# Optimization experiments

Hardware: AMD Instinct MI355X
Metric: run time of the kernel (lower is better)

The kernel has to match this reference:

```python
import jax, jax.numpy as jnp
import numpy as np

B, T, C = 2, 4096, 1024
H, M, CHUNK = 16, 64, 128
D = C // H
DELTA = 1e-6


def setup_inputs() -> dict:
    key = jax.random.key(0)
    ks = jax.random.split(key, 4)
    x = jax.random.normal(ks[0], (B, T, C), dtype=jnp.float32)
    Wqkv = jax.random.normal(ks[1], (3 * C, C), dtype=jnp.float32) * 0.02
    bqkv = jnp.zeros((3 * C,), dtype=jnp.float32)
    Wout = jax.random.normal(ks[2], (C, C), dtype=jnp.float32) * 0.02
    bout = jnp.zeros((C,), dtype=jnp.float32)
    proj = jax.random.normal(ks[3], (H, D, M), dtype=jnp.float32) / np.sqrt(D)
    return {"x": x, "Wqkv": Wqkv, "bqkv": bqkv, "Wout": Wout, "bout": bout, "proj": proj}


def reference(x, Wqkv, bqkv, Wout, bout, proj):
    b, t, c = x.shape
    qkv = x @ Wqkv.T + bqkv                      # (B,T,3C)
    q, k, v = jnp.split(qkv, 3, axis=-1)
    # (B,T,C) -> (B,H,T,D)
    def to_heads(z):
        return z.reshape(b, t, H, D).transpose(0, 2, 1, 3).astype(jnp.float32)
    q, k, v = to_heads(q), to_heads(k), to_heads(v)

    nch = t // CHUNK
    # (B,H,T,D) -> (nch, B, H, Tc, D)
    def to_chunks(z):
        return z.reshape(b, H, nch, CHUNK, D).transpose(2, 0, 1, 3, 4)
    qc, kc, vc = to_chunks(q), to_chunks(k), to_chunks(v)

    mask = jnp.tril(jnp.ones((CHUNK, CHUNK), dtype=jnp.float32))

    def step(carry, inp):
        kv_state, k_state = carry                 # (B,H,M,D), (B,H,M)
        q_ch, k_ch, v_ch = inp                    # (B,H,Tc,D)
        qp = jax.nn.relu(jnp.einsum('bhtd,hdm->bhtm', q_ch, proj))
        kp = jax.nn.relu(jnp.einsum('bhtd,hdm->bhtm', k_ch, proj))
        ctx_hist = jnp.einsum('bhtm,bhmd->bhtd', qp, kv_state)
        norm_hist = jnp.einsum('bhtm,bhm->bht', qp, k_state)
        aw = jnp.einsum('bhtm,bhsm->bhts', qp, kp) * mask  # causal intra-chunk
        ctx_intra = jnp.einsum('bhts,bhsd->bhtd', aw, v_ch)
        norm_intra = aw.sum(-1)
        out = (ctx_hist + ctx_intra) / (norm_hist + norm_intra + DELTA)[..., None]
        new_kv = kv_state + jnp.einsum('bhtm,bhtd->bhmd', kp, v_ch)
        new_k = k_state + kp.sum(2)
        return (new_kv, new_k), out

    carry0 = (jnp.zeros((b, H, M, D), jnp.float32), jnp.zeros((b, H, M), jnp.float32))
    _, outs = jax.lax.scan(step, carry0, (qc, kc, vc))  # (nch,B,H,Tc,D)
    out = outs.transpose(1, 2, 0, 3, 4).reshape(b, H, t, D)  # (B,H,T,D)
    out = out.transpose(0, 2, 1, 3).reshape(b, t, c)          # (B,T,C)
    return out @ Wout.T + bout
```

## Files before the change

### kernel.cpp

```cpp
#include <hip/hip_runtime.h>
#include <stdint.h>

#define HN 16
#define DH 64
#define MF 64
#define CHK 128
#define NCH 32
#define TSEQ 4096
#define CIN 1024
#define C3 3072

typedef __attribute__((ext_vector_type(8))) short bf16x8;
typedef __attribute__((ext_vector_type(4))) float f32x4;

__device__ __forceinline__ unsigned short f2b(float f){
  union{float f;uint32_t u;} v; v.f=f;
  return (unsigned short)((v.u + 0x7fffu + ((v.u>>16)&1u))>>16);
}

#define MFMA(a,b,c) __builtin_amdgcn_mfma_f32_16x16x32_bf16(a,b,c,0,0,0)

typedef __attribute__((address_space(1))) void gbl_t;
typedef __attribute__((address_space(3))) void lds_t;
__device__ __forceinline__ void gload_lds16(const void* g, void* l){
  __builtin_amdgcn_global_load_lds((const gbl_t*)g, (lds_t*)l, 16, 0, 0);
}

__global__ __launch_bounds__(256) void cvt_kernel(const float* __restrict__ src,
                                                  unsigned short* __restrict__ dst, int n4){
  int i = blockIdx.x*256 + threadIdx.x;
  if (i >= n4) return;
  float4 v = ((const float4*)src)[i];
  uint64_t pk = (uint64_t)f2b(v.x) | ((uint64_t)f2b(v.y)<<16)
              | ((uint64_t)f2b(v.z)<<32) | ((uint64_t)f2b(v.w)<<48);
  *(uint64_t*)(dst + (size_t)i*4) = pk;
}

__global__ __launch_bounds__(256) void projt_kernel(const float* __restrict__ proj,
                                                    unsigned short* __restrict__ projT){
  int i = blockIdx.x*256 + threadIdx.x;
  if (i >= HN*DH*MF) return;
  int h = i>>12, r = i&4095, d = r>>6, m = r&63;
  projT[(h<<12) + (m<<6) + d] = f2b(proj[i]);
}

template<int OUT_BF16, int KK>
__global__ __launch_bounds__(512, 2) void gemm8p_kernel(
    const unsigned short* __restrict__ A, const unsigned short* __restrict__ Bt,
    const float* __restrict__ bias, void* __restrict__ Cout,
    int Nn, int nbN)
{
  static_assert(KK % 128 == 0, "KK multiple of 128");
  constexpr int NT = KK / 64;
  constexpr int NI = NT / 2;
  static_assert((NT & (NT-1)) == 0, "NT pow2 for wrap");

  __shared__ unsigned short sA[2*256*64];
  __shared__ unsigned short sB[2*128*64];

  int tid = threadIdx.x;
  int w = tid>>6, l = tid&63, g = l>>4, r16 = l&15;
  int wr = w>>2, wc = w&3;

  int nwg = gridDim.x;
  int qq = nwg>>3;
  int wgid = (blockIdx.x & 7)*qq + (blockIdx.x>>3);
  int brow = (wgid / nbN)<<8;
  int bcol = (wgid % nbN)<<7;

  int rofs = tid>>3;
  int cofs = ((tid&7) ^ ((tid>>3)&7))<<3;

  const unsigned short* Ab = A + (size_t)brow*KK;
  const unsigned short* Bb = Bt + (size_t)bcol*KK;
  char* sAc = (char*)sA;
  char* sBc = (char*)sB;

  f32x4 acc[8][2];
  #pragma unroll
  for (int m=0;m<8;m++)
    #pragma unroll
    for (int n=0;n<2;n++) acc[m][n] = (f32x4){0.f,0.f,0.f,0.f};

  auto stgA = [&](int buf, int half, int kt){
    int r0 = half<<7;
    const unsigned short* gp = Ab + (size_t)(r0 + rofs)*KK + (kt<<6) + cofs;
    char* lp = sAc + (buf<<15) + (r0<<7) + (tid<<4);
    gload_lds16(gp, lp);
    gload_lds16(gp + (size_t)64*KK, lp + 8192);
  };
  auto stgB = [&](int buf, int kt){
    const unsigned short* gp = Bb + (size_t)rofs*KK + (kt<<6) + cofs;
    char* lp = sBc + (buf<<14) + (tid<<4);
    gload_lds16(gp, lp);
    gload_lds16(gp + (size_t)64*KK, lp + 8192);
  };

  bf16x8 af[4][2];
  bf16x8 bfv[2][2];

#define LDA(SAB, MH) do{                                                            \
    _Pragma("unroll")                                                               \
    for (int mf_=0; mf_<4; mf_++){                                                  \
      int row_ = wr*128 + (MH)*64 + mf_*16 + r16;                                   \
      _Pragma("unroll")                                                             \
      for (int ks_=0; ks_<2; ks_++)                                                 \
        af[mf_][ks_] = *(const bf16x8*)((SAB) + row_*128 + (((ks_*4+g)^(r16&7))<<4));\
    } }while(0)
#define LDB(SBB, NH) do{                                                            \
    int row_ = wc*32 + (NH)*16 + r16;                                               \
    _Pragma("unroll")                                                               \
    for (int ks_=0; ks_<2; ks_++)                                                   \
      bfv[NH][ks_] = *(const bf16x8*)((SBB) + row_*128 + (((ks_*4+g)^(r16&7))<<4)); \
    }while(0)
#define MM(MH, NH) do{                                                              \
    __builtin_amdgcn_s_barrier();                                                   \
    __builtin_amdgcn_sched_barrier(0);                                              \
    __builtin_amdgcn_s_setprio(1);                                                  \
    _Pragma("unroll")                                                               \
    for (int mf_=0; mf_<4; mf_++)                                                   \
      _Pragma("unroll")                                                             \
      for (int ks_=0; ks_<2; ks_++)                                                 \
        acc[(MH)*4+mf_][(NH)] = MFMA(af[mf_][ks_], bfv[NH][ks_], acc[(MH)*4+mf_][(NH)]); \
    __builtin_amdgcn_s_setprio(0);                                                  \
    __builtin_amdgcn_sched_barrier(0);                                              \
    __builtin_amdgcn_s_barrier();                                                   \
    asm volatile("" ::: "memory");                                                  \
  }while(0)
#define VM2 asm volatile("s_waitcnt vmcnt(2)" ::: "memory")

  const char* a0 = sAc;
  const char* a1 = sAc + (1<<15);
  const char* b0 = sBc;
  const char* b1 = sBc + (1<<14);

  stgA(0,0,0); stgA(0,1,0); stgB(0,0);
  stgA(1,0,1);
  VM2;
  __builtin_amdgcn_s_barrier();
  asm volatile("" ::: "memory");

  for (int it=0; it<NI; ++it){
    int to  = 2*it+1;
    int tn  = (2*it+2) & (NT-1);
    int tnn = (2*it+3) & (NT-1);
    LDA(a0,0); LDB(b0,0); stgA(1,1,to);        MM(0,0);
    LDB(b0,1);            stgB(1,to);          MM(0,1);
    LDA(a0,1);            stgA(0,0,tn);        MM(1,1);
                                         VM2;  MM(1,0);
    LDA(a1,0); LDB(b1,0); stgA(0,1,tn);        MM(0,0);
    LDB(b1,1);            stgB(0,tn);          MM(0,1);
    LDA(a1,1);            stgA(1,0,tnn);       MM(1,1);
                                         VM2;  MM(1,0);
  }
#undef LDA
#undef LDB
#undef MM
#undef VM2

  #pragma unroll
  for (int n=0;n<2;n++){
    int colg = bcol + wc*32 + n*16 + r16;
    float bv = bias[colg];
    #pragma unroll
    for (int m=0;m<8;m++){
      int rowg = brow + wr*128 + (m>>2)*64 + (m&3)*16 + g*4;
      #pragma unroll
      for (int j=0;j<4;j++){
        float v = acc[m][n][j] + bv;
        if (OUT_BF16) ((unsigned short*)Cout)[(size_t)(rowg+j)*Nn + colg] = f2b(v);
        else          ((float*)Cout)[(size_t)(rowg+j)*Nn + colg] = v;
      }
    }
  }
}

__global__ __launch_bounds__(256) void chunk_stats_kernel(
    const unsigned short* __restrict__ qkvb,
    const unsigned short* __restrict__ projT,
    float* __restrict__ Sbuf, float* __restrict__ ssum)
{
  __shared__ unsigned short s_pT[64*64];
  __shared__ unsigned short s_kpT[64*128];
  __shared__ unsigned short s_vT[64*128];
  __shared__ float s_part[256];

  int bid = blockIdx.x;
  int ch = bid&31, h = (bid>>5)&15, b = bid>>9;
  int tid = threadIdx.x, w = tid>>6, l = tid&63, g = l>>4, r16 = l&15;
  int rowbase = b*TSEQ + ch*CHK;
  const unsigned short* kg = qkvb + (size_t)rowbase*C3 + CIN   + h*DH;
  const unsigned short* vg = qkvb + (size_t)rowbase*C3 + 2*CIN + h*DH;

  {
    const unsigned short* p = projT + (h<<12);
    for (int i = tid; i < 4096; i += 256){
      int m = i>>6, d = i&63;
      *(unsigned short*)((char*)s_pT + m*128 + (((d*2) ^ ((m&7)<<4)))) = p[i];
    }
  }
  for (int i = tid; i < 1024; i += 256){
    int t = i>>3, d0 = (i&7)<<3;
    bf16x8 vv = *(const bf16x8*)(vg + (size_t)t*C3 + d0);
    #pragma unroll
    for (int j=0;j<8;j++){
      int d = d0+j;
      *(unsigned short*)((char*)s_vT + d*256 + (((t*2) ^ ((d&15)<<4)))) = (unsigned short)vv[j];
    }
  }
  __syncthreads();

  f32x4 kacc[2][4];
  #pragma unroll
  for (int tr=0;tr<2;tr++)
    #pragma unroll
    for (int nc=0;nc<4;nc++) kacc[tr][nc] = (f32x4){0.f,0.f,0.f,0.f};
  #pragma unroll
  for (int ks=0; ks<2; ks++){
    bf16x8 a[2];
    #pragma unroll
    for (int tr=0;tr<2;tr++){
      int t = w*32 + tr*16 + r16;
      a[tr] = *(const bf16x8*)(kg + (size_t)t*C3 + ks*32 + g*8);
    }
    #pragma unroll
    for (int nc=0;nc<4;nc++){
      int m = nc*16 + r16;
      bf16x8 bb = *(const bf16x8*)((const char*)s_pT + m*128 + (((ks*64 + g*16) ^ ((m&7)<<4))));
      #pragma unroll
      for (int tr=0;tr<2;tr++)
        kacc[tr][nc] = MFMA(a[tr], bb, kacc[tr][nc]);
    }
  }
  #pragma unroll
  for (int nc=0;nc<4;nc++){
    float v = 0.f;
    #pragma unroll
    for (int tr=0;tr<2;tr++)
      #pragma unroll
      for (int j=0;j<4;j++){
        float x = kacc[tr][nc][j]; x = x>0.f?x:0.f;
        v += x;
        int t = w*32 + tr*16 + g*4 + j;
        int m = nc*16 + r16;
        *(unsigned short*)((char*)s_kpT + m*256 + (((t*2) ^ ((m&15)<<4)))) = f2b(x);
      }
    v += __shfl_xor(v,16); v += __shfl_xor(v,32);
    if (g==0) s_part[w*64 + nc*16 + r16] = v;
  }
  __syncthreads();

  f32x4 sacc[4];
  #pragma unroll
  for (int dc=0;dc<4;dc++) sacc[dc] = (f32x4){0.f,0.f,0.f,0.f};
  int mrow = w*16 + r16;
  #pragma unroll
  for (int ks=0; ks<4; ks++){
    bf16x8 a = *(const bf16x8*)((const char*)s_kpT + mrow*256 + (((ks*64 + g*16) ^ ((mrow&15)<<4))));
    #pragma unroll
    for (int dc=0; dc<4; dc++){
      int d = dc*16 + r16;
      bf16x8 bb = *(const bf16x8*)((const char*)s_vT + d*256 + (((ks*64 + g*16) ^ ((d&15)<<4))));
      sacc[dc] = MFMA(a, bb, sacc[dc]);
    }
  }
  float* So = Sbuf + ((size_t)((b*HN + h)*NCH + ch))*4096;
  #pragma unroll
  for (int dc=0; dc<4; dc++)
    #pragma unroll
    for (int j=0;j<4;j++)
      So[(w*16 + g*4 + j)*64 + dc*16 + r16] = sacc[dc][j];
  if (tid < 64){
    float v = s_part[tid] + s_part[64+tid] + s_part[128+tid] + s_part[192+tid];
    ssum[((size_t)((b*HN + h)*NCH + ch))*64 + tid] = v;
  }
}

__global__ __launch_bounds__(256) void scan_kernel(
  const float* __restrict__ Sbuf, const float* __restrict__ ssum,
  float* __restrict__ kvstate, float* __restrict__ kstate)
{
  int bh = blockIdx.x>>2, qd = blockIdx.x&3, tid = threadIdx.x;
  const float4* Sp = (const float4*)(Sbuf + (size_t)bh*NCH*4096);
  float4* kvp = (float4*)(kvstate + (size_t)bh*NCH*4096);
  int idx0 = (tid>>2)*16 + qd*4 + (tid&3);
  float4 acc = make_float4(0.f,0.f,0.f,0.f);
  for (int c2=0; c2<NCH; c2++){
    int idx = c2*1024 + idx0;
    float4 s = Sp[idx];
    kvp[idx] = acc;
    acc.x += s.x; acc.y += s.y; acc.z += s.z; acc.w += s.w;
  }
  if (qd==0 && tid < 64){
    float a = 0.f;
    const float* sp = ssum + (size_t)bh*NCH*64;
    float* kp2 = kstate + (size_t)bh*NCH*64;
    for (int c2=0;c2<NCH;c2++){ kp2[c2*64+tid] = a; a += sp[c2*64+tid]; }
  }
}

__global__ __launch_bounds__(256) void chunk_out_kernel(
    const unsigned short* __restrict__ qkvb,
    const unsigned short* __restrict__ projT,
    const float* __restrict__ kvstate,
    const float* __restrict__ kstate,
    unsigned short* __restrict__ attnb)
{
  __shared__ unsigned short s_qp[128*64];
  __shared__ unsigned short s_kp[128*64];
  __shared__ unsigned short s_vT[64*128];
  __shared__ unsigned short s_pa[64*64];

  int bid = blockIdx.x;
  int ch = bid&31, h=(bid>>5)&15, b=bid>>9;
  int tid=threadIdx.x, w=tid>>6, l=tid&63, g=l>>4, r16=l&15;
  int rowbase = b*TSEQ + ch*CHK;
  const unsigned short* qg = qkvb + (size_t)rowbase*C3 + h*DH;
  const unsigned short* kg = qg + CIN;
  const unsigned short* vg = qg + 2*CIN;
  const float* kvg = kvstate + ((size_t)((b*HN+h)*NCH + ch))*4096;
  const float* ksg = kstate  + ((size_t)((b*HN+h)*NCH + ch))*64;

  {
    const unsigned short* p = projT + (h<<12);
    for (int i = tid; i < 4096; i += 256){
      int m = i>>6, d = i&63;
      *(unsigned short*)((char*)s_pa + m*128 + (((d*2) ^ ((m&7)<<4)))) = p[i];
    }
  }
  for (int i = tid; i < 1024; i += 256){
    int t = i>>3, d0 = (i&7)<<3;
    bf16x8 vv = *(const bf16x8*)(vg + (size_t)t*C3 + d0);
    #pragma unroll
    for (int j=0;j<8;j++){
      int d = d0+j;
      *(unsigned short*)((char*)s_vT + d*256 + (((t*2) ^ ((d&15)<<4)))) = (unsigned short)vv[j];
    }
  }
  __syncthreads();

  f32x4 qacc[2][4];
  #pragma unroll
  for (int tr=0;tr<2;tr++)
    #pragma unroll
    for (int nc=0;nc<4;nc++) qacc[tr][nc] = (f32x4){0.f,0.f,0.f,0.f};
  #pragma unroll
  for (int ks=0; ks<2; ks++){
    bf16x8 a[2];
    #pragma unroll
    for (int tr=0;tr<2;tr++){
      int t = w*32 + tr*16 + r16;
      a[tr] = *(const bf16x8*)(qg + (size_t)t*C3 + ks*32 + g*8);
    }
    #pragma unroll
    for (int nc=0;nc<4;nc++){
      int m = nc*16 + r16;
      bf16x8 bb = *(const bf16x8*)((const char*)s_pa + m*128 + (((ks*64 + g*16) ^ ((m&7)<<4))));
      #pragma unroll
      for (int tr=0;tr<2;tr++)
        qacc[tr][nc] = MFMA(a[tr], bb, qacc[tr][nc]);
    }
  }
  float nh[2][4];
  #pragma unroll
  for (int tr=0;tr<2;tr++)
    #pragma unroll
    for (int j=0;j<4;j++) nh[tr][j] = 0.f;
  #pragma unroll
  for (int nc=0;nc<4;nc++){
    float ksv = ksg[nc*16 + r16];
    #pragma unroll
    for (int tr=0;tr<2;tr++)
      #pragma unroll
      for (int j=0;j<4;j++){
        float x = qacc[tr][nc][j]; x = x>0.f?x:0.f;
        nh[tr][j] += x*ksv;
        int t = w*32 + tr*16 + g*4 + j;
        int m = nc*16 + r16;
        *(unsigned short*)((char*)s_qp + t*128 + (((m*2) ^ ((t&7)<<4)))) = f2b(x);
      }
  }
  f32x4 kacc[2][4];
  #pragma unroll
  for (int tr=0;tr<2;tr++)
    #pragma unroll
    for (int nc=0;nc<4;nc++) kacc[tr][nc] = (f32x4){0.f,0.f,0.f,0.f};
  #pragma unroll
  for (int ks=0; ks<2; ks++){
    bf16x8 a[2];
    #pragma unroll
    for (int tr=0;tr<2;tr++){
      int t = w*32 + tr*16 + r16;
      a[tr] = *(const bf16x8*)(kg + (size_t)t*C3 + ks*32 + g*8);
    }
    #pragma unroll
    for (int nc=0;nc<4;nc++){
      int m = nc*16 + r16;
      bf16x8 bb = *(const bf16x8*)((const char*)s_pa + m*128 + (((ks*64 + g*16) ^ ((m&7)<<4))));
      #pragma unroll
      for (int tr=0;tr<2;tr++)
        kacc[tr][nc] = MFMA(a[tr], bb, kacc[tr][nc]);
    }
  }
  #pragma unroll
  for (int nc=0;nc<4;nc++)
    #pragma unroll
    for (int tr=0;tr<2;tr++)
      #pragma unroll
      for (int j=0;j<4;j++){
        float x = kacc[tr][nc][j]; x = x>0.f?x:0.f;
        int t = w*32 + tr*16 + g*4 + j;
        int m = nc*16 + r16;
        *(unsigned short*)((char*)s_kp + t*128 + (((m*2) ^ ((t&7)<<4)))) = f2b(x);
      }
  __syncthreads();

  f32x4 ctx[2][4];
  float ni[2][4];
  #pragma unroll
  for (int tr=0;tr<2;tr++){
    #pragma unroll
    for (int dc=0;dc<4;dc++) ctx[tr][dc] = (f32x4){0.f,0.f,0.f,0.f};
    #pragma unroll
    for (int j=0;j<4;j++) ni[tr][j] = 0.f;
  }

  for (int sb=0; sb<4; sb++){
    f32x4 aw[2][2];
    #pragma unroll
    for (int tr=0;tr<2;tr++)
      #pragma unroll
      for (int sc=0;sc<2;sc++) aw[tr][sc] = (f32x4){0.f,0.f,0.f,0.f};
    #pragma unroll
    for (int ks=0; ks<2; ks++){
      bf16x8 a[2];
      #pragma unroll
      for (int tr=0;tr<2;tr++){
        int t = w*32 + tr*16 + r16;
        a[tr] = *(const bf16x8*)((const char*)s_qp + t*128 + (((ks*64 + g*16) ^ ((t&7)<<4))));
      }
      #pragma unroll
      for (int sc=0;sc<2;sc++){
        int s = sb*32 + sc*16 + r16;
        bf16x8 bb = *(const bf16x8*)((const char*)s_kp + s*128 + (((ks*64 + g*16) ^ ((s&7)<<4))));
        #pragma unroll
        for (int tr=0;tr<2;tr++)
          aw[tr][sc] = MFMA(a[tr], bb, aw[tr][sc]);
      }
    }
    #pragma unroll
    for (int tr=0;tr<2;tr++)
      #pragma unroll
      for (int sc=0;sc<2;sc++)
        #pragma unroll
        for (int j=0;j<4;j++){
          int t = w*32 + tr*16 + g*4 + j;
          int s = sb*32 + sc*16 + r16;
          float x = (s<=t)? aw[tr][sc][j] : 0.f;
          ni[tr][j] += x;
          int sl = sc*16 + r16;
          *(unsigned short*)((char*)s_pa + t*64 + (((sl*2) ^ ((t&3)<<4)))) = f2b(x);
        }
    __syncthreads();
    #pragma unroll
    for (int tr=0;tr<2;tr++){
      int t = w*32 + tr*16 + r16;
      bf16x8 a2 = *(const bf16x8*)((const char*)s_pa + t*64 + (((g*16) ^ ((t&3)<<4))));
      #pragma unroll
      for (int dc=0;dc<4;dc++){
        int d = dc*16 + r16;
        bf16x8 bb = *(const bf16x8*)((const char*)s_vT + d*256 + (((sb*64 + g*16) ^ ((d&15)<<4))));
        ctx[tr][dc] = MFMA(a2, bb, ctx[tr][dc]);
      }
    }
    __syncthreads();
  }

  #pragma unroll
  for (int ks=0; ks<2; ks++){
    bf16x8 a[2];
    #pragma unroll
    for (int tr=0;tr<2;tr++){
      int t = w*32 + tr*16 + r16;
      a[tr] = *(const bf16x8*)((const char*)s_qp + t*128 + (((ks*64 + g*16) ^ ((t&7)<<4))));
    }
    #pragma unroll
    for (int dc=0;dc<4;dc++){
      bf16x8 bb;
      #pragma unroll
      for (int i=0;i<8;i++)
        bb[i] = (short)f2b(kvg[(ks*32 + g*8 + i)*64 + dc*16 + r16]);
      #pragma unroll
      for (int tr=0;tr<2;tr++)
        ctx[tr][dc] = MFMA(a[tr], bb, ctx[tr][dc]);
    }
  }

  float nrm[2][4];
  #pragma unroll
  for (int tr=0;tr<2;tr++)
    #pragma unroll
    for (int j=0;j<4;j++){
      float v = nh[tr][j] + ni[tr][j];
      v += __shfl_xor(v,1); v += __shfl_xor(v,2);
      v += __shfl_xor(v,4); v += __shfl_xor(v,8);
      nrm[tr][j] = v + 1e-6f;
    }

  #pragma unroll
  for (int tr=0;tr<2;tr++)
    #pragma unroll
    for (int dc=0;dc<4;dc++)
      #pragma unroll
      for (int j=0;j<4;j++){
        int t = w*32 + tr*16 + g*4 + j;
        int d = dc*16 + r16;
        attnb[(size_t)(rowbase + t)*CIN + h*DH + d] = f2b(ctx[tr][dc][j] / nrm[tr][j]);
      }
}

extern "C" void kernel_launch(void* const* d_in, const int* in_sizes, int n_in,
                              void* d_out, int out_size, void* d_ws, size_t ws_size,
                              hipStream_t stream)
{
  const float* x    = (const float*)d_in[0];
  const float* Wqkv = (const float*)d_in[1];
  const float* bqkv = (const float*)d_in[2];
  const float* Wout = (const float*)d_in[3];
  const float* bout = (const float*)d_in[4];
  const float* proj = (const float*)d_in[5];

  char* ws = (char*)d_ws;
  unsigned short* xb     = (unsigned short*)(ws + 0);
  unsigned short* attnb  = (unsigned short*)(ws + 0);
  unsigned short* wqkvb  = (unsigned short*)(ws + 16777216);
  float*          ssum   = (float*)(ws + 16777216);
  float*          kstate = (float*)(ws + 17039360);
  unsigned short* qkvb   = (unsigned short*)(ws + 23068672);
  unsigned short* woutb  = (unsigned short*)(ws + 73400320);
  unsigned short* projTb = (unsigned short*)(ws + 75497472);
  float*          Sbuf   = (float*)(ws + 75628544);
  float*          kvstate= (float*)(ws + 92405760);

  cvt_kernel<<<8192, 256, 0, stream>>>(x, xb, 2097152);
  cvt_kernel<<<3072, 256, 0, stream>>>(Wqkv, wqkvb, 786432);
  cvt_kernel<<<1024, 256, 0, stream>>>(Wout, woutb, 262144);
  projt_kernel<<<256, 256, 0, stream>>>(proj, projTb);

  gemm8p_kernel<1,1024><<<768, 512, 0, stream>>>(xb, wqkvb, bqkv, qkvb, 3072, 24);

  chunk_stats_kernel<<<1024, 256, 0, stream>>>(qkvb, projTb, Sbuf, ssum);
  scan_kernel<<<128, 256, 0, stream>>>(Sbuf, ssum, kvstate, kstate);
  chunk_out_kernel<<<1024, 256, 0, stream>>>(qkvb, projTb, kvstate, kstate, attnb);

  gemm8p_kernel<0,1024><<<256, 512, 0, stream>>>(attnb, woutb, bout, d_out, 1024, 8);
}
```

Before: 164.5 us.

## Widen GEMM block tile to 256x256 for more operand reuse

The GEMM block tile grows from 256x128 to 256x256. Each wave now computes a 128x64 output with 32 accumulator fragments, and the B staging is split into two halves with a reworked load/wait schedule. The goal is higher arithmetic intensity per LDS load and less global traffic for B. In exchange the kernel uses more registers and LDS, which hurts occupancy, and the grid halves (384 and 128 blocks), leaving the output projection with fewer blocks than the 256 CUs.

```diff
diff --git a/kernel.cpp b/kernel.cpp
--- a/kernel.cpp
+++ b/kernel.cpp
@@ -56,7 +56,7 @@
   static_assert((NT & (NT-1)) == 0, "NT pow2 for wrap");
 
   __shared__ unsigned short sA[2*256*64];
-  __shared__ unsigned short sB[2*128*64];
+  __shared__ unsigned short sB[2*256*64];
 
   int tid = threadIdx.x;
   int w = tid>>6, l = tid&63, g = l>>4, r16 = l&15;
@@ -66,7 +66,7 @@
   int qq = nwg>>3;
   int wgid = (blockIdx.x & 7)*qq + (blockIdx.x>>3);
   int brow = (wgid / nbN)<<8;
-  int bcol = (wgid % nbN)<<7;
+  int bcol = (wgid % nbN)<<8;
 
   int rofs = tid>>3;
   int cofs = ((tid&7) ^ ((tid>>3)&7))<<3;
@@ -76,67 +76,68 @@
   char* sAc = (char*)sA;
   char* sBc = (char*)sB;
 
-  f32x4 acc[8][2];
+  f32x4 acc[8][4];
   #pragma unroll
   for (int m=0;m<8;m++)
     #pragma unroll
-    for (int n=0;n<2;n++) acc[m][n] = (f32x4){0.f,0.f,0.f,0.f};
+    for (int n=0;n<4;n++) acc[m][n] = (f32x4){0.f,0.f,0.f,0.f};
 
   auto stgA = [&](int buf, int half, int kt){
-    int r0 = half<<7;
-    const unsigned short* gp = Ab + (size_t)(r0 + rofs)*KK + (kt<<6) + cofs;
-    char* lp = sAc + (buf<<15) + (r0<<7) + (tid<<4);
+    const unsigned short* gp = Ab + (size_t)(half*128 + rofs)*KK + ((size_t)kt<<6) + cofs;
+    char* lp = sAc + (buf<<15) + (half<<14) + (tid<<4);
     gload_lds16(gp, lp);
     gload_lds16(gp + (size_t)64*KK, lp + 8192);
   };
-  auto stgB = [&](int buf, int kt){
-    const unsigned short* gp = Bb + (size_t)rofs*KK + (kt<<6) + cofs;
-    char* lp = sBc + (buf<<14) + (tid<<4);
+  auto stgB = [&](int buf, int half, int kt){
+    const unsigned short* gp = Bb + (size_t)(half*128 + rofs)*KK + ((size_t)kt<<6) + cofs;
+    char* lp = sBc + (buf<<15) + (half<<14) + (tid<<4);
     gload_lds16(gp, lp);
     gload_lds16(gp + (size_t)64*KK, lp + 8192);
   };
 
   bf16x8 af[4][2];
-  bf16x8 bfv[2][2];
-
-#define LDA(SAB, MH) do{                                                            \
-    _Pragma("unroll")                                                               \
-    for (int mf_=0; mf_<4; mf_++){                                                  \
-      int row_ = wr*128 + (MH)*64 + mf_*16 + r16;                                   \
-      _Pragma("unroll")                                                             \
-      for (int ks_=0; ks_<2; ks_++)                                                 \
-        af[mf_][ks_] = *(const bf16x8*)((SAB) + row_*128 + (((ks_*4+g)^(r16&7))<<4));\
+  bf16x8 bf[2][2][2];
+
+#define LDA(BUF, MH) do{                                                             \
+    _Pragma("unroll")                                                                \
+    for (int mf_=0; mf_<4; mf_++){                                                   \
+      int rr_ = wr*128 + (MH)*64 + mf_*16 + r16;                                     \
+      _Pragma("unroll")                                                              \
+      for (int ks_=0; ks_<2; ks_++)                                                  \
+        af[mf_][ks_] = *(const bf16x8*)(sAc + ((BUF)<<15) + rr_*128 +                \
+                                        (((ks_*4+g)^(r16&7))<<4));                   \
     } }while(0)
-#define LDB(SBB, NH) do{                                                            \
-    int row_ = wc*32 + (NH)*16 + r16;                                               \
-    _Pragma("unroll")                                                               \
-    for (int ks_=0; ks_<2; ks_++)                                                   \
-      bfv[NH][ks_] = *(const bf16x8*)((SBB) + row_*128 + (((ks_*4+g)^(r16&7))<<4)); \
-    }while(0)
-#define MM(MH, NH) do{                                                              \
-    __builtin_amdgcn_s_barrier();                                                   \
-    __builtin_amdgcn_sched_barrier(0);                                              \
-    __builtin_amdgcn_s_setprio(1);                                                  \
-    _Pragma("unroll")                                                               \
-    for (int mf_=0; mf_<4; mf_++)                                                   \
-      _Pragma("unroll")                                                             \
-      for (int ks_=0; ks_<2; ks_++)                                                 \
-        acc[(MH)*4+mf_][(NH)] = MFMA(af[mf_][ks_], bfv[NH][ks_], acc[(MH)*4+mf_][(NH)]); \
-    __builtin_amdgcn_s_setprio(0);                                                  \
-    __builtin_amdgcn_sched_barrier(0);                                              \
-    __builtin_amdgcn_s_barrier();                                                   \
-    asm volatile("" ::: "memory");                                                  \
+#define LDB(BUF, NH) do{                                                             \
+    _Pragma("unroll")                                                                \
+    for (int nf_=0; nf_<2; nf_++){                                                   \
+      int rb_ = wc*64 + (NH)*32 + nf_*16 + r16;                                      \
+      _Pragma("unroll")                                                              \
+      for (int ks_=0; ks_<2; ks_++)                                                  \
+        bf[NH][nf_][ks_] = *(const bf16x8*)(sBc + ((BUF)<<15) + rb_*128 +            \
+                                            (((ks_*4+g)^(r16&7))<<4));               \
+    } }while(0)
+#define MM(MH, NH) do{                                                               \
+    __builtin_amdgcn_s_barrier();                                                    \
+    __builtin_amdgcn_sched_barrier(0);                                               \
+    __builtin_amdgcn_s_setprio(1);                                                   \
+    _Pragma("unroll")                                                                \
+    for (int mf_=0; mf_<4; mf_++)                                                    \
+      _Pragma("unroll")                                                              \
+      for (int nf_=0; nf_<2; nf_++)                                                  \
+        _Pragma("unroll")                                                            \
+        for (int ks_=0; ks_<2; ks_++)                                                \
+          acc[(MH)*4+mf_][(NH)*2+nf_] =                                              \
+            MFMA(af[mf_][ks_], bf[NH][nf_][ks_], acc[(MH)*4+mf_][(NH)*2+nf_]);       \
+    __builtin_amdgcn_s_setprio(0);                                                   \
+    __builtin_amdgcn_sched_barrier(0);                                               \
+    __builtin_amdgcn_s_barrier();                                                    \
+    asm volatile("" ::: "memory");                                                   \
   }while(0)
-#define VM2 asm volatile("s_waitcnt vmcnt(2)" ::: "memory")
-
-  const char* a0 = sAc;
-  const char* a1 = sAc + (1<<15);
-  const char* b0 = sBc;
-  const char* b1 = sBc + (1<<14);
-
-  stgA(0,0,0); stgA(0,1,0); stgB(0,0);
-  stgA(1,0,1);
-  VM2;
+#define VM4 asm volatile("s_waitcnt vmcnt(4)" ::: "memory")
+
+  stgA(0,0,0); stgA(0,1,0); stgB(0,0,0); stgB(0,1,0);
+  stgB(1,0,1); stgA(1,0,1);
+  VM4;
   __builtin_amdgcn_s_barrier();
   asm volatile("" ::: "memory");
 
@@ -144,23 +145,23 @@
     int to  = 2*it+1;
     int tn  = (2*it+2) & (NT-1);
     int tnn = (2*it+3) & (NT-1);
-    LDA(a0,0); LDB(b0,0); stgA(1,1,to);        MM(0,0);
-    LDB(b0,1);            stgB(1,to);          MM(0,1);
-    LDA(a0,1);            stgA(0,0,tn);        MM(1,1);
-                                         VM2;  MM(1,0);
-    LDA(a1,0); LDB(b1,0); stgA(0,1,tn);        MM(0,0);
-    LDB(b1,1);            stgB(0,tn);          MM(0,1);
-    LDA(a1,1);            stgA(1,0,tnn);       MM(1,1);
-                                         VM2;  MM(1,0);
+    LDA(0,0); LDB(0,0); stgA(1,1,to);        MM(0,0);
+    LDB(0,1);           stgB(1,1,to);        MM(0,1);
+    LDA(0,1);           stgB(0,0,tn);        MM(1,1);
+                        stgA(0,0,tn);  VM4;  MM(1,0);
+    LDA(1,0); LDB(1,0); stgA(0,1,tn);        MM(0,0);
+    LDB(1,1);           stgB(0,1,tn);        MM(0,1);
+    LDA(1,1);           stgB(1,0,tnn);       MM(1,1);
+                        stgA(1,0,tnn); VM4;  MM(1,0);
   }
 #undef LDA
 #undef LDB
 #undef MM
-#undef VM2
-
-  #pragma unroll
-  for (int n=0;n<2;n++){
-    int colg = bcol + wc*32 + n*16 + r16;
+#undef VM4
+
+  #pragma unroll
+  for (int n=0;n<4;n++){
+    int colg = bcol + wc*64 + (n>>1)*32 + (n&1)*16 + r16;
     float bv = bias[colg];
     #pragma unroll
     for (int m=0;m<8;m++){
@@ -547,11 +548,11 @@
   cvt_kernel<<<1024, 256, 0, stream>>>(Wout, woutb, 262144);
   projt_kernel<<<256, 256, 0, stream>>>(proj, projTb);
 
-  gemm8p_kernel<1,1024><<<768, 512, 0, stream>>>(xb, wqkvb, bqkv, qkvb, 3072, 24);
+  gemm8p_kernel<1,1024><<<384, 512, 0, stream>>>(xb, wqkvb, bqkv, qkvb, 3072, 12);
 
   chunk_stats_kernel<<<1024, 256, 0, stream>>>(qkvb, projTb, Sbuf, ssum);
   scan_kernel<<<128, 256, 0, stream>>>(Sbuf, ssum, kvstate, kstate);
   chunk_out_kernel<<<1024, 256, 0, stream>>>(qkvb, projTb, kvstate, kstate, attnb);
 
-  gemm8p_kernel<0,1024><<<256, 512, 0, stream>>>(attnb, woutb, bout, d_out, 1024, 8);
-}
+  gemm8p_kernel<0,1024><<<128, 512, 0, stream>>>(attnb, woutb, bout, d_out, 1024, 4);
+}
```

Result: slower. 175.5 us (+6.7%).
